# Kernel optimization log

Hardware: AMD Instinct MI355X
Metric: run time of the kernel (lower is better)

The kernel has to match this reference:

```python
import jax, jax.numpy as jnp
import numpy as np

N_QUBITS = 20
N_PART = 10  # log2(out_features=1024)
W_MUL = (2.0 ** 0.5) * (5.0 ** -0.5)  # he_std * lrmul with gain=sqrt(2), lrmul=1

_H = (jnp.array([[1.0, 1.0], [1.0, -1.0]], dtype=jnp.complex64) / jnp.sqrt(jnp.array(2.0, jnp.float32)))


def _rx(theta):
    c = jnp.cos(theta * 0.5).astype(jnp.complex64)
    s = (-1j * jnp.sin(theta * 0.5)).astype(jnp.complex64)
    return jnp.stack([jnp.stack([c, s]), jnp.stack([s, c])])


def _ry(theta):
    c = jnp.cos(theta * 0.5).astype(jnp.complex64)
    s = jnp.sin(theta * 0.5).astype(jnp.complex64)
    return jnp.stack([jnp.stack([c, -s]), jnp.stack([s, c])])


def _rz(theta):
    e = jnp.exp(-0.5j * theta.astype(jnp.complex64))
    z = jnp.zeros((), jnp.complex64)
    return jnp.stack([jnp.stack([e, z]), jnp.stack([z, jnp.conj(e)])])


def _apply_1q(state, gate, q):
    # Apply 2x2 gate on qubit q (qubit 0 = most significant bit, matching kron order).
    s = state.reshape(2 ** q, 2, -1)
    return jnp.einsum('ab,ibj->iaj', gate, s).reshape(-1)


def _apply_cnot(state, c, t, n):
    a, b = (c, t) if c < t else (t, c)
    s = state.reshape(2 ** a, 2, 2 ** (b - a - 1), 2, 2 ** (n - b - 1))
    if c < t:
        # control at axis 1; after slicing, target is axis 2
        s = s.at[:, 1].set(jnp.flip(s[:, 1], axis=2))
    else:
        # control at axis 3; after slicing, target is axis 1
        s = s.at[:, :, :, 1].set(jnp.flip(s[:, :, :, 1], axis=1))
    return s.reshape(-1)


def setup_inputs() -> dict:
    key = jax.random.key(0)
    kx, kw = jax.random.split(key)
    x = jax.random.normal(kx, (1, N_QUBITS), dtype=jnp.float32)
    weight = jax.random.uniform(kw, (3 * N_QUBITS,), dtype=jnp.float32,
                                minval=0.0, maxval=2.0 * np.pi)
    return {"x": x, "weight": weight}


def reference(x, weight):
    n = N_QUBITS
    xq = jnp.squeeze(x)  # (n_qubits,)
    state = jnp.zeros(2 ** n, dtype=jnp.complex64).at[0].set(1.0 + 0j)
    # encoding layer: H, ry(arctan(x)), rz(arctan(x^2)) on each qubit
    for q in range(n):
        state = _apply_1q(state, _H, q)
        state = _apply_1q(state, _ry(jnp.arctan(xq[q])), q)
        state = _apply_1q(state, _rz(jnp.arctan(xq[q] * xq[q])), q)
    # variational layer: ring of CNOTs (q -> q+1, q -> q+2), then rx,rz,rx
    w = weight * W_MUL
    for q in range(n):
        state = _apply_cnot(state, q, (q + 1) % n, n)
        state = _apply_cnot(state, q, (q + 2) % n, n)
    for q in range(n):
        state = _apply_1q(state, _rx(w[3 * q + 0]), q)
        state = _apply_1q(state, _rz(w[3 * q + 1]), q)
        state = _apply_1q(state, _rx(w[3 * q + 2]), q)
    # partial measurement of the first N_PART (most significant) qubits:
    # marginalize |amp|^2 over the remaining qubits
    probs = (jnp.abs(state) ** 2).astype(jnp.float32)
    hidden = probs.reshape(2 ** N_PART, -1).sum(axis=1)
    return hidden[None, :]  # (1, 2**N_PART)
```

## Files before the change

### kernel.cpp

```cpp
#include <hip/hip_runtime.h>
#include <cstdint>


#define NQ      20
#define NPART   10
#define NH      1024
#define BLOCK   256
#define NSLICE  32

struct MaskArg { uint32_t m[NQ]; };

__device__ __forceinline__ float2 cmul(float2 a, float2 b) {
    return make_float2(fmaf(a.x, b.x, -a.y * b.y), fmaf(a.x, b.y, a.y * b.x));
}
__device__ __forceinline__ float2 cadd(float2 a, float2 b) {
    return make_float2(a.x + b.x, a.y + b.y);
}

__global__ __launch_bounds__(BLOCK, 4) void qulinear_kernel(
        const float* __restrict__ x, const float* __restrict__ w,
        float* __restrict__ ws, MaskArg masks) {
    __shared__ float2 v[NQ][2];
    __shared__ float2 U[NPART][2][2];
    __shared__ float2 ex[4][4][64];

    const int tid = threadIdx.x;

    if (tid < NQ) {
        float xq = x[tid];
        float th = atanf(xq);
        float ph = atanf(xq * xq);
        float c, s, cp, sp;
        __sincosf(0.5f * th, &s, &c);
        __sincosf(0.5f * ph, &sp, &cp);
        float a = (c - s) * 0.70710678118654752f;
        float b = (c + s) * 0.70710678118654752f;
        v[tid][0] = make_float2(a * cp, -a * sp);
        v[tid][1] = make_float2(b * cp,  b * sp);
    }
    if (tid < NPART) {
        const float WM = 0.63245553203367590f;
        float a0 = w[3 * tid + 0] * WM;
        float a1 = w[3 * tid + 1] * WM;
        float a2 = w[3 * tid + 2] * WM;
        float c0, s0, c1, s1, c2, s2;
        __sincosf(0.5f * a0, &s0, &c0);
        __sincosf(0.5f * a1, &s1, &c1);
        __sincosf(0.5f * a2, &s2, &c2);
        float2 e0 = make_float2(c1, -s1), e1 = make_float2(c1, s1);
        float2 m00 = cmul(e0, make_float2(c0, 0.f));
        float2 m01 = cmul(e0, make_float2(0.f, -s0));
        float2 m10 = cmul(e1, make_float2(0.f, -s0));
        float2 m11 = cmul(e1, make_float2(c0, 0.f));
        float2 r00 = make_float2(c2, 0.f), r01 = make_float2(0.f, -s2);
        U[tid][0][0] = cadd(cmul(r00, m00), cmul(r01, m10));
        U[tid][0][1] = cadd(cmul(r00, m01), cmul(r01, m11));
        U[tid][1][0] = cadd(cmul(r01, m00), cmul(r00, m10));
        U[tid][1][1] = cadd(cmul(r01, m01), cmul(r00, m11));
    }
    __syncthreads();

    const int wq   = tid >> 6;
    const int lane = tid & 63;
    const uint32_t l = blockIdx.x;

    const uint32_t y0 = ((uint32_t)lane << NPART) | l | ((uint32_t)wq << 18);
    uint32_t sbase = 0, d16 = 0, d17 = 0;
    #pragma unroll
    for (int q = 0; q < NQ; ++q) {
        sbase |= (uint32_t)(__popc(masks.m[q] & y0) & 1) << q;
        d16   |= (uint32_t)((masks.m[q] >> 16) & 1u) << q;
        d17   |= (uint32_t)((masks.m[q] >> 17) & 1u) << q;
    }
    uint32_t s[4];
    s[0] = sbase; s[1] = sbase ^ d16; s[2] = sbase ^ d17; s[3] = sbase ^ d16 ^ d17;

    float2 g[4];
    #pragma unroll
    for (int j = 0; j < 4; ++j)
        g[j] = cmul(U[0][wq >> 1][j >> 1], U[1][wq & 1][j & 1]);

    float2 amp[4];
    #pragma unroll
    for (int r = 0; r < 4; ++r) amp[r] = make_float2(1.f, 0.f);

    #pragma unroll
    for (int q = 0; q < NQ; ++q) {
        float2 v0 = v[q][0], v1 = v[q][1];
        #pragma unroll
        for (int r = 0; r < 4; ++r) {
            bool b = (s[r] >> q) & 1u;
            float2 sel = make_float2(b ? v1.x : v0.x, b ? v1.y : v0.y);
            amp[r] = cmul(amp[r], sel);
        }
    }

    {
        float2 g00 = U[3][0][0], g01 = U[3][0][1], g10 = U[3][1][0], g11 = U[3][1][1];
        float2 a, b;
        a = amp[0]; b = amp[1];
        amp[0] = cadd(cmul(g00, a), cmul(g01, b));
        amp[1] = cadd(cmul(g10, a), cmul(g11, b));
        a = amp[2]; b = amp[3];
        amp[2] = cadd(cmul(g00, a), cmul(g01, b));
        amp[3] = cadd(cmul(g10, a), cmul(g11, b));
    }
    {
        float2 g00 = U[2][0][0], g01 = U[2][0][1], g10 = U[2][1][0], g11 = U[2][1][1];
        float2 a, b;
        a = amp[0]; b = amp[2];
        amp[0] = cadd(cmul(g00, a), cmul(g01, b));
        amp[2] = cadd(cmul(g10, a), cmul(g11, b));
        a = amp[1]; b = amp[3];
        amp[1] = cadd(cmul(g00, a), cmul(g01, b));
        amp[3] = cadd(cmul(g10, a), cmul(g11, b));
    }

    #pragma unroll
    for (int p = 0; p < 6; ++p) {
        const int lm = 1 << p;
        const bool bit = (lane & lm) != 0;
        float2 g00 = U[9 - p][0][0], g01 = U[9 - p][0][1];
        float2 g10 = U[9 - p][1][0], g11 = U[9 - p][1][1];
        float2 ga = bit ? g11 : g00;
        float2 gb = bit ? g10 : g01;
        #pragma unroll
        for (int r = 0; r < 4; ++r) {
            float2 mine = amp[r];
            float2 oth = make_float2(__shfl_xor(mine.x, lm, 64),
                                     __shfl_xor(mine.y, lm, 64));
            amp[r] = cadd(cmul(ga, mine), cmul(gb, oth));
        }
    }

    #pragma unroll
    for (int r = 0; r < 4; ++r) ex[wq][r][lane] = amp[r];
    __syncthreads();
    #pragma unroll
    for (int r = 0; r < 4; ++r) {
        float2 acc = cmul(g[0], ex[0][r][lane]);
        acc = cadd(acc, cmul(g[1], ex[1][r][lane]));
        acc = cadd(acc, cmul(g[2], ex[2][r][lane]));
        acc = cadd(acc, cmul(g[3], ex[3][r][lane]));
        amp[r] = acc;
    }

    float* wsp = ws + (size_t)(blockIdx.x & (NSLICE - 1)) * NH;
    #pragma unroll
    for (int r = 0; r < 4; ++r) {
        int h = (wq << 8) | (r << 6) | lane;
        atomicAdd(&wsp[h], fmaf(amp[r].x, amp[r].x, amp[r].y * amp[r].y));
    }
}

__global__ __launch_bounds__(BLOCK) void reduce_kernel(
        const float* __restrict__ ws, float* __restrict__ out) {
    int h = blockIdx.x * BLOCK + threadIdx.x;
    float acc = 0.f;
    #pragma unroll
    for (int s = 0; s < NSLICE; ++s) acc += ws[s * NH + h];
    out[h] = acc;
}

extern "C" void kernel_launch(void* const* d_in, const int* in_sizes, int n_in,
                              void* d_out, int out_size, void* d_ws, size_t ws_size,
                              hipStream_t stream) {
    const float* x = (const float*)d_in[0];
    const float* w = (const float*)d_in[1];
    float* out = (float*)d_out;

    MaskArg ma;
    {
        uint32_t M[NQ];
        for (int q = 0; q < NQ; ++q) M[q] = 1u << q;
        for (int q = NQ - 1; q >= 0; --q) {
            M[(q + 2) % NQ] ^= M[q];
            M[(q + 1) % NQ] ^= M[q];
        }
        for (int q = 0; q < NQ; ++q) {
            uint32_t im = 0;
            for (int j = 0; j < NQ; ++j)
                if ((M[q] >> j) & 1) im |= 1u << (NQ - 1 - j);
            ma.m[q] = im;
        }
    }

    hipMemsetAsync(d_ws, 0, (size_t)NSLICE * NH * sizeof(float), stream);
    qulinear_kernel<<<NH, BLOCK, 0, stream>>>(x, w, (float*)d_ws, ma);
    reduce_kernel<<<NH / BLOCK, BLOCK, 0, stream>>>((const float*)d_ws, out);
}
```

Measured before the change: 67.37 us.

## Replace atomic slice accumulation with per-block writes and tree reduce; pair qubit factors

Each block now writes its own 1024-float row of partial probabilities with plain stores instead of atomically adding into 32 shared slices. This drops the memset and the atomic contention. The reduce kernel is rewritten to sum 1024 rows using 64 blocks with a shared-memory two-stage reduction. Per-qubit amplitude factors are premultiplied into 4-entry pair tables, which halves the product loop. The cost is a 4 MB workspace that must be written and read back.

```diff
diff --git a/kernel.cpp b/kernel.cpp
--- a/kernel.cpp
+++ b/kernel.cpp
@@ -6,7 +6,7 @@
 #define NPART   10
 #define NH      1024
 #define BLOCK   256
-#define NSLICE  32
+#define NPAIR   10
 
 struct MaskArg { uint32_t m[NQ]; };
 
@@ -22,6 +22,7 @@
         float* __restrict__ ws, MaskArg masks) {
     __shared__ float2 v[NQ][2];
     __shared__ float2 U[NPART][2][2];
+    __shared__ float2 P[NPAIR][4];
     __shared__ float2 ex[4][4][64];
 
     const int tid = threadIdx.x;
@@ -59,6 +60,11 @@
         U[tid][1][1] = cadd(cmul(r01, m01), cmul(r00, m11));
     }
     __syncthreads();
+    if (tid < 4 * NPAIR) {
+        int p = tid >> 2, j = tid & 3;
+        P[p][j] = cmul(v[2 * p][j & 1], v[2 * p + 1][(j >> 1) & 1]);
+    }
+    __syncthreads();
 
     const int wq   = tid >> 6;
     const int lane = tid & 63;
@@ -82,16 +88,14 @@
 
     float2 amp[4];
     #pragma unroll
-    for (int r = 0; r < 4; ++r) amp[r] = make_float2(1.f, 0.f);
-
-    #pragma unroll
-    for (int q = 0; q < NQ; ++q) {
-        float2 v0 = v[q][0], v1 = v[q][1];
+    for (int r = 0; r < 4; ++r) amp[r] = P[0][s[r] & 3];
+
+    #pragma unroll
+    for (int p = 1; p < NPAIR; ++p) {
         #pragma unroll
         for (int r = 0; r < 4; ++r) {
-            bool b = (s[r] >> q) & 1u;
-            float2 sel = make_float2(b ? v1.x : v0.x, b ? v1.y : v0.y);
-            amp[r] = cmul(amp[r], sel);
+            int idx = (s[r] >> (2 * p)) & 3;
+            amp[r] = cmul(amp[r], P[p][idx]);
         }
     }
 
@@ -145,21 +149,32 @@
         amp[r] = acc;
     }
 
-    float* wsp = ws + (size_t)(blockIdx.x & (NSLICE - 1)) * NH;
+    float* wsp = ws + (size_t)blockIdx.x * NH;
     #pragma unroll
     for (int r = 0; r < 4; ++r) {
         int h = (wq << 8) | (r << 6) | lane;
-        atomicAdd(&wsp[h], fmaf(amp[r].x, amp[r].x, amp[r].y * amp[r].y));
+        wsp[h] = fmaf(amp[r].x, amp[r].x, amp[r].y * amp[r].y);
     }
 }
 
 __global__ __launch_bounds__(BLOCK) void reduce_kernel(
         const float* __restrict__ ws, float* __restrict__ out) {
-    int h = blockIdx.x * BLOCK + threadIdx.x;
+    __shared__ float red[16][17];
+    const int g  = blockIdx.x;
+    const int hl = threadIdx.x & 15;
+    const int rg = threadIdx.x >> 4;
+    const float* p = ws + (size_t)(rg * 64) * NH + g * 16 + hl;
     float acc = 0.f;
     #pragma unroll
-    for (int s = 0; s < NSLICE; ++s) acc += ws[s * NH + h];
-    out[h] = acc;
+    for (int k = 0; k < 64; ++k) acc += p[(size_t)k * NH];
+    red[rg][hl] = acc;
+    __syncthreads();
+    if (threadIdx.x < 16) {
+        float a = 0.f;
+        #pragma unroll
+        for (int i = 0; i < 16; ++i) a += red[i][threadIdx.x];
+        out[g * 16 + threadIdx.x] = a;
+    }
 }
 
 extern "C" void kernel_launch(void* const* d_in, const int* in_sizes, int n_in,
@@ -185,7 +200,6 @@
         }
     }
 
-    hipMemsetAsync(d_ws, 0, (size_t)NSLICE * NH * sizeof(float), stream);
     qulinear_kernel<<<NH, BLOCK, 0, stream>>>(x, w, (float*)d_ws, ma);
-    reduce_kernel<<<NH / BLOCK, BLOCK, 0, stream>>>((const float*)d_ws, out);
-}
+    reduce_kernel<<<NH / 16, BLOCK, 0, stream>>>((const float*)d_ws, out);
+}
```

Result: no change. 66.10 us (-1.9%).
